# Kernel tuning notes

Measured on AMD Instinct MI355X. Metric: run time of the kernel, lower is better.

## Reference

```python
import jax, jax.numpy as jnp
import numpy as np

DIM = 64
HEADS = 8
DIM_HEAD = 64
INNER = HEADS * DIM_HEAD  # 512
MLP = 256
DEPTH = 4
B = 64
HW = 15
NPATCH = HW * HW  # 225
N = NPATCH + 1    # 226 tokens incl cls
SCALE = DIM_HEAD ** -0.5
EPS = 1e-5


def setup_inputs() -> dict:
    key = jax.random.key(0)
    ks = jax.random.split(key, 20)
    s = 0.02
    inp = {
        "hsi": jax.random.normal(ks[0], (B, DIM, HW, HW), jnp.float32),
        "lidar": jax.random.normal(ks[1], (B, DIM, HW, HW), jnp.float32),
        "cls_hsi": jax.random.normal(ks[2], (1, 1, DIM), jnp.float32),
        "cls_lidar": jax.random.normal(ks[3], (1, 1, DIM), jnp.float32),
        "pos_hsi": jax.random.normal(ks[4], (1, N, DIM), jnp.float32),
        "pos_lidar": jax.random.normal(ks[5], (1, N, DIM), jnp.float32),
        "fmg_w": jax.random.normal(ks[6], (2 * DIM, DIM * DIM), jnp.float32) * s,
        "ln1_g": jnp.ones((DEPTH, DIM), jnp.float32),
        "ln1_b": jnp.zeros((DEPTH, DIM), jnp.float32),
        "qkv_w": jax.random.normal(ks[7], (DEPTH, DIM, 3 * INNER), jnp.float32) * s,
        "out_w": jax.random.normal(ks[8], (DEPTH, INNER, DIM), jnp.float32) * s,
        "out_b": jnp.zeros((DEPTH, DIM), jnp.float32),
        "ln2_g": jnp.ones((DEPTH, DIM), jnp.float32),
        "ln2_b": jnp.zeros((DEPTH, DIM), jnp.float32),
        "ff_w1": jax.random.normal(ks[9], (DEPTH, DIM, MLP), jnp.float32) * s,
        "ff_b1": jnp.zeros((DEPTH, MLP), jnp.float32),
        "ff_w2": jax.random.normal(ks[10], (DEPTH, MLP, DIM), jnp.float32) * s,
        "ff_b2": jnp.zeros((DEPTH, DIM), jnp.float32),
    }
    return inp


def _ln(x, g, b):
    m = x.mean(-1, keepdims=True)
    v = ((x - m) ** 2).mean(-1, keepdims=True)
    return (x - m) * jax.lax.rsqrt(v + EPS) * g + b


def _attn(x, dfm, g, b, wqkv, wo, bo):
    # x: [B, N, DIM]; dfm: [B, DIM_HEAD] diagonal of per-sample fusion matrix
    xn = _ln(x, g, b)
    qkv = xn @ wqkv  # [B, N, 3*INNER]
    q, k, v = jnp.split(qkv, 3, axis=-1)
    def heads(t):
        return t.reshape(B, N, HEADS, DIM_HEAD).transpose(0, 2, 1, 3)  # bhnd
    q, v = heads(q), heads(v)
    # torch.einsum('bhnd,bdd->bhnd', q, fm): repeated 'd' in bdd = diagonal of fm
    k = q * dfm[:, None, None, :]
    dots = jnp.einsum('bhid,bhjd->bhij', q, k) * SCALE
    attn = jax.nn.softmax(dots, axis=-1)
    out = jnp.einsum('bhij,bhjd->bhid', attn, v)
    out = out.transpose(0, 2, 1, 3).reshape(B, N, INNER)
    return out @ wo + bo


def _ff(x, g, b, w1, b1, w2, b2):
    xn = _ln(x, g, b)
    h = jax.nn.gelu(xn @ w1 + b1, approximate=False)
    return h @ w2 + b2


def reference(hsi, lidar, cls_hsi, cls_lidar, pos_hsi, pos_lidar, fmg_w,
              ln1_g, ln1_b, qkv_w, out_w, out_b, ln2_g, ln2_b,
              ff_w1, ff_b1, ff_w2, ff_b2):
    # patch_to_embedding with p1=p2=1: b c h w -> b (h w) c
    h_e = hsi.reshape(B, DIM, NPATCH).transpose(0, 2, 1)
    l_e = lidar.reshape(B, DIM, NPATCH).transpose(0, 2, 1)

    # fusion matrix from pre-exchange embeddings
    x = jnp.concatenate([h_e.mean(1), l_e.mean(1)], axis=-1)  # [B, 2*DIM]
    fm = jax.nn.sigmoid(x @ fmg_w).reshape(B, DIM, DIM)
    dfm = jnp.diagonal(fm, axis1=1, axis2=2)  # [B, DIM]

    # _exchange_embedding (faithful to source: reads both halves from hsi)
    n2 = NPATCH // 2
    h_ex = jnp.concatenate([h_e[:, :n2], h_e[:, n2:]], axis=1)
    l_ex = jnp.concatenate([h_e[:, :n2], h_e[:, n2:]], axis=1)

    h_ex = jnp.concatenate([jnp.broadcast_to(cls_hsi, (B, 1, DIM)), h_ex], axis=1)
    l_ex = jnp.concatenate([jnp.broadcast_to(cls_lidar, (B, 1, DIM)), l_ex], axis=1)
    h_ex = h_ex + pos_hsi[:, :N]
    l_ex = l_ex + pos_lidar[:, :N]

    def run_layers(h, l):
        for i in range(DEPTH):
            h = _attn(h, dfm, ln1_g[i], ln1_b[i], qkv_w[i], out_w[i], out_b[i]) + h
            h = _ff(h, ln2_g[i], ln2_b[i], ff_w1[i], ff_b1[i], ff_w2[i], ff_b2[i]) + h
            l = _attn(l, dfm, ln1_g[i], ln1_b[i], qkv_w[i], out_w[i], out_b[i]) + l
            l = _ff(l, ln2_g[i], ln2_b[i], ff_w1[i], ff_b1[i], ff_w2[i], ff_b2[i]) + l
        return h, l

    h_ex, l_ex = run_layers(h_ex, l_ex)

    # _exchange_token: swap cls tokens
    h_new = jnp.concatenate([l_ex[:, :1], h_ex[:, 1:]], axis=1)
    l_new = jnp.concatenate([h_ex[:, :1], l_ex[:, 1:]], axis=1)

    h_new, l_new = run_layers(h_new, l_new)
    return h_new[:, 0] + l_new[:, 0]
```

## Files before the change

### kernel.cpp

```cpp
#include <hip/hip_runtime.h>
#include <hip/hip_bf16.h>
#include <cstdint>

#define NB 64
#define ND 64
#define NH 8
#define DH 64
#define NIN 512
#define NMLP 256
#define NDEPTH 4
#define NPATCH 225
#define NTOK 226
#define NSB 128
#define NROWS (NSB*NTOK)

#define VP 240

typedef __attribute__((ext_vector_type(8))) short bfrag8;
typedef __attribute__((ext_vector_type(4))) float ffrag4;

__device__ __forceinline__ unsigned short f2b(float f) {
  __hip_bfloat16 h = __float2bfloat16(f);
  unsigned short u; __builtin_memcpy(&u, &h, 2); return u;
}

__global__ void k_dfm(const float* __restrict__ hsi, const float* __restrict__ lidar,
                      const float* __restrict__ fmg_w, float* __restrict__ sdfm) {
  __shared__ float xc[128];
  int b = blockIdx.x, t = threadIdx.x;
  const float* src = (t < 64) ? hsi : lidar;
  int d = t & 63;
  const float* p = src + ((size_t)b * 64 + d) * NPATCH;
  float s = 0.f;
  for (int i = 0; i < NPATCH; ++i) s += p[i];
  xc[t] = s * (1.0f / 225.0f);
  __syncthreads();
  if (t < 64) {
    float acc = 0.f;
    const float* w = fmg_w + t * 65;
    for (int c = 0; c < 128; ++c) acc += xc[c] * w[c * 4096];
    float sg = 1.0f / (1.0f + expf(-acc));
    sdfm[b * 64 + t] = sqrtf(sg);
  }
}

__global__ void k_build(const float* __restrict__ hsi,
                        const float* __restrict__ cls_h, const float* __restrict__ cls_l,
                        const float* __restrict__ pos_h, const float* __restrict__ pos_l,
                        const float* __restrict__ g, const float* __restrict__ bb,
                        float* __restrict__ X, uint16_t* __restrict__ Xn) {
  int r = blockIdx.x;
  int sb = r / NTOK, n = r - sb * NTOK;
  int s = sb >> 6, b = sb & 63;
  int d = threadIdx.x;
  float v;
  if (n == 0) v = s ? cls_l[d] : cls_h[d];
  else        v = hsi[((size_t)b * 64 + d) * NPATCH + (n - 1)];
  v += (s ? pos_l : pos_h)[n * ND + d];
  X[(size_t)r * ND + d] = v;
  float sm = v, sq = v * v;
  #pragma unroll
  for (int o = 32; o; o >>= 1) { sm += __shfl_xor(sm, o); sq += __shfl_xor(sq, o); }
  float m = sm * (1.f / 64.f);
  float rs = rsqrtf(sq * (1.f / 64.f) - m * m + 1e-5f);
  Xn[(size_t)r * ND + d] = f2b((v - m) * rs * g[d] + bb[d]);
}

__global__ __launch_bounds__(256) void k_wconv(
    const float* __restrict__ qkv_w, const float* __restrict__ out_w,
    const float* __restrict__ ff_w1, const float* __restrict__ ff_w2,
    uint16_t* __restrict__ Wqv, uint16_t* __restrict__ Wo,
    uint16_t* __restrict__ W1, uint16_t* __restrict__ W2) {
  int i = blockIdx.x * 256 + threadIdx.x;
  if (i < 262144) {
    int ly = i >> 16, rem = i & 65535, n = rem >> 6, k = rem & 63;
    int col = n + ((n >> 9) << 9);
    Wqv[i] = f2b(qkv_w[((size_t)ly * 64 + k) * 1536 + col]);
  } else if (i < 393216) {
    int j = i - 262144;
    int ly = j >> 15, rem = j & 32767, n = rem >> 9, k = rem & 511;
    Wo[j] = f2b(out_w[((size_t)ly * 512 + k) * 64 + n]);
  } else if (i < 458752) {
    int j = i - 393216;
    int ly = j >> 14, rem = j & 16383, n = rem >> 6, k = rem & 63;
    W1[j] = f2b(ff_w1[((size_t)ly * 64 + k) * 256 + n]);
  } else {
    int j = i - 458752;
    int ly = j >> 14, rem = j & 16383, n = rem >> 8, k = rem & 255;
    W2[j] = f2b(ff_w2[((size_t)ly * 256 + k) * 64 + n]);
  }
}

__global__ __launch_bounds__(256) void k_fattn(const uint16_t* __restrict__ Xn,
    const uint16_t* __restrict__ Wqv,
    const float* __restrict__ sdfm, uint16_t* __restrict__ Og) {
  __shared__ __align__(16) uint16_t qs[240 * 64];
  __shared__ __align__(16) uint16_t vt[64 * VP];
  __shared__ __align__(16) uint16_t pb[4][512];
  int bh = blockIdx.x;
  int sb = bh >> 3, h = bh & 7;
  int t = threadIdx.x, w = t >> 6, l = t & 63;
  int quad = l >> 4, c = l & 15;
  const uint16_t* Xb = Xn + (size_t)sb * NTOK * ND;

  float sf[4];
  #pragma unroll
  for (int dt = 0; dt < 4; ++dt)
    sf[dt] = sdfm[(sb & 63) * 64 + dt * 16 + c] * 0.35355339059327373f;

  for (int it = w; it < 15; it += 4) {
    int i0 = it * 16;
    int ri = i0 + c; if (ri > 225) ri = 225;
    bfrag8 a0 = *(const bfrag8*)(Xb + (size_t)ri * 64 + quad * 8);
    bfrag8 a1 = *(const bfrag8*)(Xb + (size_t)ri * 64 + 32 + quad * 8);
    #pragma unroll
    for (int dt = 0; dt < 4; ++dt) {
      int nq = h * 64 + dt * 16 + c;
      bfrag8 bq0 = *(const bfrag8*)(Wqv + (size_t)nq * 64 + quad * 8);
      bfrag8 bq1 = *(const bfrag8*)(Wqv + (size_t)nq * 64 + 32 + quad * 8);
      ffrag4 zq = {0.f, 0.f, 0.f, 0.f};
      zq = __builtin_amdgcn_mfma_f32_16x16x32_bf16(a0, bq0, zq, 0, 0, 0);
      zq = __builtin_amdgcn_mfma_f32_16x16x32_bf16(a1, bq1, zq, 0, 0, 0);
      bfrag8 bv0 = *(const bfrag8*)(Wqv + (size_t)(512 + nq) * 64 + quad * 8);
      bfrag8 bv1 = *(const bfrag8*)(Wqv + (size_t)(512 + nq) * 64 + 32 + quad * 8);
      ffrag4 zv = {0.f, 0.f, 0.f, 0.f};
      zv = __builtin_amdgcn_mfma_f32_16x16x32_bf16(a0, bv0, zv, 0, 0, 0);
      zv = __builtin_amdgcn_mfma_f32_16x16x32_bf16(a1, bv1, zv, 0, 0, 0);
      int d = dt * 16 + c;
      #pragma unroll
      for (int r = 0; r < 4; ++r) {
        int i = i0 + quad * 4 + r;
        qs[i * 64 + ((((d >> 3) ^ (i & 7))) << 3) + (d & 7)] = f2b(zq[r] * sf[dt]);
        vt[d * VP + i] = f2b(zv[r]);
      }
    }
  }
  __syncthreads();

  uint16_t* pw = &pb[w][0];
  for (int it = w; it < 15; it += 4) {
    int i0 = it * 16;
    int ra = i0 + c, sa = ra & 7;
    bfrag8 a0 = *(const bfrag8*)(qs + ra * 64 + ((quad ^ sa) << 3));
    bfrag8 a1 = *(const bfrag8*)(qs + ra * 64 + (((quad + 4) ^ sa) << 3));
    ffrag4 acc[15];
    #pragma unroll
    for (int jt = 0; jt < 15; ++jt) {
      int rb = jt * 16 + c, sk = rb & 7;
      bfrag8 b0 = *(const bfrag8*)(qs + rb * 64 + ((quad ^ sk) << 3));
      bfrag8 b1 = *(const bfrag8*)(qs + rb * 64 + (((quad + 4) ^ sk) << 3));
      ffrag4 z = {0.f, 0.f, 0.f, 0.f};
      z = __builtin_amdgcn_mfma_f32_16x16x32_bf16(a0, b0, z, 0, 0, 0);
      z = __builtin_amdgcn_mfma_f32_16x16x32_bf16(a1, b1, z, 0, 0, 0);
      acc[jt] = z;
    }
    float rinv[4];
    #pragma unroll
    for (int r = 0; r < 4; ++r) {
      float m = -1e30f;
      #pragma unroll
      for (int jt = 0; jt < 15; ++jt) m = fmaxf(m, acc[jt][r]);
      #pragma unroll
      for (int o = 8; o; o >>= 1) m = fmaxf(m, __shfl_xor(m, o));
      float s = 0.f;
      #pragma unroll
      for (int jt = 0; jt < 15; ++jt) {
        float p = __expf(acc[jt][r] - m);
        if (jt == 14 && c >= 2) p = 0.f;
        acc[jt][r] = p;
        s += p;
      }
      #pragma unroll
      for (int o = 8; o; o >>= 1) s += __shfl_xor(s, o);
      rinv[r] = 1.f / s;
    }
    ffrag4 oa[4];
    #pragma unroll
    for (int dt = 0; dt < 4; ++dt) oa[dt] = (ffrag4){0.f, 0.f, 0.f, 0.f};
    for (int jc = 0; jc < 8; ++jc) {
      if (jc == 7) {
        *(uint64_t*)(pw + c * 32 + 16 + quad * 4) = 0ull;
      }
      #pragma unroll
      for (int r = 0; r < 4; ++r) {
        int row = quad * 4 + r;
        pw[row * 32 + c] = f2b(acc[2 * jc][r] * rinv[r]);
        if (jc < 7) pw[row * 32 + 16 + c] = f2b(acc[2 * jc + 1][r] * rinv[r]);
      }
      bfrag8 pa = *(const bfrag8*)(pw + c * 32 + quad * 8);
      int j0 = jc * 32;
      #pragma unroll
      for (int dt = 0; dt < 4; ++dt) {
        bfrag8 vb;
        if (jc < 7)
          vb = *(const bfrag8*)(vt + (dt * 16 + c) * VP + j0 + quad * 8);
        else
          vb = *(const bfrag8*)(vt + (dt * 16 + c) * VP + 224 + (quad & 1) * 8);
        oa[dt] = __builtin_amdgcn_mfma_f32_16x16x32_bf16(pa, vb, oa[dt], 0, 0, 0);
      }
    }
    #pragma unroll
    for (int dt = 0; dt < 4; ++dt) {
      #pragma unroll
      for (int r = 0; r < 4; ++r) {
        int i = i0 + quad * 4 + r;
        if (i < NTOK)
          Og[((size_t)sb * NTOK + i) * NIN + h * DH + dt * 16 + c] = f2b(oa[dt][r]);
      }
    }
  }
}

__global__ __launch_bounds__(256) void k_proj(const uint16_t* __restrict__ Og,
    const uint16_t* __restrict__ Wot,
    const float* __restrict__ bo, float* __restrict__ X,
    const float* __restrict__ g2, const float* __restrict__ bb2,
    uint16_t* __restrict__ Xn2) {
  int t = threadIdx.x, w = t >> 6, l = t & 63;
  int quad = l >> 4, c = l & 15;
  int r0 = blockIdx.x * 64;
  const uint16_t* orow = Og + (size_t)(r0 + w * 16 + c) * 512 + quad * 8;
  bfrag8 a[16];
  #pragma unroll
  for (int kc = 0; kc < 16; ++kc) a[kc] = *(const bfrag8*)(orow + kc * 32);
  ffrag4 acc[4];
  #pragma unroll
  for (int jt = 0; jt < 4; ++jt) acc[jt] = (ffrag4){0.f, 0.f, 0.f, 0.f};
  #pragma unroll
  for (int kc = 0; kc < 16; ++kc) {
    #pragma unroll
    for (int jt = 0; jt < 4; ++jt) {
      bfrag8 b = *(const bfrag8*)(Wot + (size_t)(jt * 16 + c) * 512 + kc * 32 + quad * 8);
      acc[jt] = __builtin_amdgcn_mfma_f32_16x16x32_bf16(a[kc], b, acc[jt], 0, 0, 0);
    }
  }
  float xv[4][4];
  #pragma unroll
  for (int jt = 0; jt < 4; ++jt) {
    float bv = bo[jt * 16 + c];
    #pragma unroll
    for (int r = 0; r < 4; ++r) {
      int il = w * 16 + quad * 4 + r;
      size_t idx = (size_t)(r0 + il) * 64 + jt * 16 + c;
      float v = X[idx] + acc[jt][r] + bv;
      X[idx] = v;
      xv[jt][r] = v;
    }
  }
  #pragma unroll
  for (int r = 0; r < 4; ++r) {
    float s = xv[0][r] + xv[1][r] + xv[2][r] + xv[3][r];
    float q = xv[0][r]*xv[0][r] + xv[1][r]*xv[1][r] + xv[2][r]*xv[2][r] + xv[3][r]*xv[3][r];
    #pragma unroll
    for (int o = 8; o; o >>= 1) { s += __shfl_xor(s, o); q += __shfl_xor(q, o); }
    float m = s * (1.f / 64.f);
    float rs = rsqrtf(q * (1.f / 64.f) - m * m + 1e-5f);
    int il = w * 16 + quad * 4 + r;
    #pragma unroll
    for (int jt = 0; jt < 4; ++jt) {
      int n = jt * 16 + c;
      Xn2[(size_t)(r0 + il) * 64 + n] = f2b((xv[jt][r] - m) * rs * g2[n] + bb2[n]);
    }
  }
}

__global__ __launch_bounds__(256) void k_ff(float* __restrict__ X,
    const uint16_t* __restrict__ Xn2,
    const uint16_t* __restrict__ W1t,
    const float* __restrict__ b1,
    const uint16_t* __restrict__ W2t,
    const float* __restrict__ b2,
    const float* __restrict__ gn, const float* __restrict__ bbn,
    uint16_t* __restrict__ XnOut) {
  __shared__ __align__(16) uint16_t ha[4][16 * 264];
  int t = threadIdx.x, w = t >> 6, l = t & 63;
  int quad = l >> 4, c = l & 15;
  int r0 = blockIdx.x * 64;
  const uint16_t* xrow = Xn2 + (size_t)(r0 + w * 16 + c) * 64;
  bfrag8 a0 = *(const bfrag8*)(xrow + quad * 8);
  bfrag8 a1 = *(const bfrag8*)(xrow + 32 + quad * 8);
  ffrag4 acc[16];
  #pragma unroll
  for (int jt = 0; jt < 16; ++jt) {
    bfrag8 b0  = *(const bfrag8*)(W1t + (size_t)(jt * 16 + c) * 64 + quad * 8);
    bfrag8 b1f = *(const bfrag8*)(W1t + (size_t)(jt * 16 + c) * 64 + 32 + quad * 8);
    ffrag4 z = {0.f, 0.f, 0.f, 0.f};
    z = __builtin_amdgcn_mfma_f32_16x16x32_bf16(a0, b0, z, 0, 0, 0);
    z = __builtin_amdgcn_mfma_f32_16x16x32_bf16(a1, b1f, z, 0, 0, 0);
    acc[jt] = z;
  }
  uint16_t* haw = &ha[w][0];
  #pragma unroll
  for (int jt = 0; jt < 16; ++jt) {
    float bv = b1[jt * 16 + c];
    #pragma unroll
    for (int r = 0; r < 4; ++r) {
      float z = acc[jt][r] + bv;
      float hg = 0.5f * z * (1.f + erff(z * 0.7071067811865476f));
      haw[(quad * 4 + r) * 264 + jt * 16 + c] = f2b(hg);
    }
  }
  __syncthreads();
  ffrag4 o2[4];
  #pragma unroll
  for (int jt = 0; jt < 4; ++jt) o2[jt] = (ffrag4){0.f, 0.f, 0.f, 0.f};
  #pragma unroll
  for (int kc = 0; kc < 8; ++kc) {
    bfrag8 pa = *(const bfrag8*)(haw + c * 264 + kc * 32 + quad * 8);
    #pragma unroll
    for (int jt = 0; jt < 4; ++jt) {
      bfrag8 vb = *(const bfrag8*)(W2t + (size_t)(jt * 16 + c) * 256 + kc * 32 + quad * 8);
      o2[jt] = __builtin_amdgcn_mfma_f32_16x16x32_bf16(pa, vb, o2[jt], 0, 0, 0);
    }
  }
  float xv[4][4];
  #pragma unroll
  for (int jt = 0; jt < 4; ++jt) {
    float bv = b2[jt * 16 + c];
    #pragma unroll
    for (int r = 0; r < 4; ++r) {
      int il = w * 16 + quad * 4 + r;
      size_t idx = (size_t)(r0 + il) * 64 + jt * 16 + c;
      float v = X[idx] + o2[jt][r] + bv;
      X[idx] = v;
      xv[jt][r] = v;
    }
  }
  #pragma unroll
  for (int r = 0; r < 4; ++r) {
    float s = xv[0][r] + xv[1][r] + xv[2][r] + xv[3][r];
    float q = xv[0][r]*xv[0][r] + xv[1][r]*xv[1][r] + xv[2][r]*xv[2][r] + xv[3][r]*xv[3][r];
    #pragma unroll
    for (int o = 8; o; o >>= 1) { s += __shfl_xor(s, o); q += __shfl_xor(q, o); }
    float m = s * (1.f / 64.f);
    float rs = rsqrtf(q * (1.f / 64.f) - m * m + 1e-5f);
    int il = w * 16 + quad * 4 + r;
    #pragma unroll
    for (int jt = 0; jt < 4; ++jt) {
      int n = jt * 16 + c;
      XnOut[(size_t)(r0 + il) * 64 + n] = f2b((xv[jt][r] - m) * rs * gn[n] + bbn[n]);
    }
  }
}

__global__ void k_xchg(float* __restrict__ X, uint16_t* __restrict__ Xn,
                       const float* __restrict__ g, const float* __restrict__ bb) {
  int b = blockIdx.x, d = threadIdx.x;
  size_t i0 = (size_t)(b * NTOK) * ND + d;
  size_t i1 = (size_t)((64 + b) * NTOK) * ND + d;
  float a = X[i0], cc = X[i1];
  X[i0] = cc; X[i1] = a;
  float s0 = cc, q0 = cc * cc, s1 = a, q1 = a * a;
  #pragma unroll
  for (int o = 32; o; o >>= 1) {
    s0 += __shfl_xor(s0, o); q0 += __shfl_xor(q0, o);
    s1 += __shfl_xor(s1, o); q1 += __shfl_xor(q1, o);
  }
  float m0 = s0 * (1.f / 64.f), rs0 = rsqrtf(q0 * (1.f / 64.f) - m0 * m0 + 1e-5f);
  float m1 = s1 * (1.f / 64.f), rs1 = rsqrtf(q1 * (1.f / 64.f) - m1 * m1 + 1e-5f);
  Xn[i0] = f2b((cc - m0) * rs0 * g[d] + bb[d]);
  Xn[i1] = f2b((a - m1) * rs1 * g[d] + bb[d]);
}

__global__ void k_out(const float* __restrict__ X, float* __restrict__ out) {
  int i = blockIdx.x * 64 + threadIdx.x;
  int b = i >> 6, d = i & 63;
  out[i] = X[(size_t)b * NTOK * ND + d] + X[(size_t)(64 + b) * NTOK * ND + d];
}

extern "C" void kernel_launch(void* const* d_in, const int* in_sizes, int n_in,
                              void* d_out, int out_size, void* d_ws, size_t ws_size,
                              hipStream_t stream) {
  const float* hsi   = (const float*)d_in[0];
  const float* lidar = (const float*)d_in[1];
  const float* cls_h = (const float*)d_in[2];
  const float* cls_l = (const float*)d_in[3];
  const float* pos_h = (const float*)d_in[4];
  const float* pos_l = (const float*)d_in[5];
  const float* fmg_w = (const float*)d_in[6];
  const float* ln1_g = (const float*)d_in[7];
  const float* ln1_b = (const float*)d_in[8];
  const float* qkv_w = (const float*)d_in[9];
  const float* out_w = (const float*)d_in[10];
  const float* out_b = (const float*)d_in[11];
  const float* ln2_g = (const float*)d_in[12];
  const float* ln2_b = (const float*)d_in[13];
  const float* ff_w1 = (const float*)d_in[14];
  const float* ff_b1 = (const float*)d_in[15];
  const float* ff_w2 = (const float*)d_in[16];
  const float* ff_b2 = (const float*)d_in[17];

  char* ws = (char*)d_ws;
  float*    X    = (float*)ws;
  float*    sdfm = (float*)(ws + 7405568);
  uint16_t* Xn   = (uint16_t*)(ws + 7421952);
  uint16_t* Xn2  = (uint16_t*)(ws + 11124736);
  uint16_t* Og   = (uint16_t*)(ws + 14827520);
  uint16_t* Wqv  = (uint16_t*)(ws + 44449792);
  uint16_t* Wo   = (uint16_t*)(ws + 44974080);
  uint16_t* W1   = (uint16_t*)(ws + 45236224);
  uint16_t* W2   = (uint16_t*)(ws + 45367296);

  k_wconv<<<2048, 256, 0, stream>>>(qkv_w, out_w, ff_w1, ff_w2, Wqv, Wo, W1, W2);
  k_dfm<<<NB, 128, 0, stream>>>(hsi, lidar, fmg_w, sdfm);
  k_build<<<NROWS, 64, 0, stream>>>(hsi, cls_h, cls_l, pos_h, pos_l,
                                    ln1_g, ln1_b, X, Xn);
  for (int pass = 0; pass < 2; ++pass) {
    for (int ly = 0; ly < NDEPTH; ++ly) {
      int nx = (ly + 1) & 3;
      k_fattn<<<NSB * NH, 256, 0, stream>>>(Xn, Wqv + (size_t)ly * 65536, sdfm, Og);
      k_proj<<<452, 256, 0, stream>>>(Og, Wo + (size_t)ly * 32768, out_b + ly * ND,
                                      X, ln2_g + ly * ND, ln2_b + ly * ND, Xn2);
      k_ff<<<452, 256, 0, stream>>>(X, Xn2,
                                    W1 + (size_t)ly * 16384, ff_b1 + ly * NMLP,
                                    W2 + (size_t)ly * 16384, ff_b2 + ly * ND,
                                    ln1_g + nx * ND, ln1_b + nx * ND, Xn);
    }
    if (pass == 0) k_xchg<<<64, 64, 0, stream>>>(X, Xn, ln1_g, ln1_b);
  }
  k_out<<<64, 64, 0, stream>>>(X, (float*)d_out);
}
```

Before: 897.8 us.

## Transpose V MFMA, pad V tile, defer softmax normalization, cheaper bf16 convert

The V projection now uses swapped MFMA operands so each lane writes four consecutive d-rows for one token, and the V row pitch grows to 248 so LDS bank conflicts on the transposed store drop. The Q tile shrinks to 226 rows with clamped reads, and the pad columns of V are zeroed explicitly. Softmax normalization moves from every probability element to the final output, and the float-to-bf16 conversion becomes an inline bit-twiddle round-to-nearest-even that does not handle NaN. Together these target LDS traffic and per-element ALU work in the fused attention kernel.

```diff
diff --git a/kernel.cpp b/kernel.cpp
--- a/kernel.cpp
+++ b/kernel.cpp
@@ -14,14 +14,15 @@
 #define NSB 128
 #define NROWS (NSB*NTOK)
 
-#define VP 240
+#define VP 248
 
 typedef __attribute__((ext_vector_type(8))) short bfrag8;
 typedef __attribute__((ext_vector_type(4))) float ffrag4;
 
 __device__ __forceinline__ unsigned short f2b(float f) {
-  __hip_bfloat16 h = __float2bfloat16(f);
-  unsigned short u; __builtin_memcpy(&u, &h, 2); return u;
+  uint32_t u; __builtin_memcpy(&u, &f, 4);
+  u += 0x7fff + ((u >> 16) & 1);
+  return (unsigned short)(u >> 16);
 }
 
 __global__ void k_dfm(const float* __restrict__ hsi, const float* __restrict__ lidar,
@@ -94,7 +95,7 @@
 __global__ __launch_bounds__(256) void k_fattn(const uint16_t* __restrict__ Xn,
     const uint16_t* __restrict__ Wqv,
     const float* __restrict__ sdfm, uint16_t* __restrict__ Og) {
-  __shared__ __align__(16) uint16_t qs[240 * 64];
+  __shared__ __align__(16) uint16_t qs[226 * 64];
   __shared__ __align__(16) uint16_t vt[64 * VP];
   __shared__ __align__(16) uint16_t pb[4][512];
   int bh = blockIdx.x;
@@ -110,9 +111,10 @@
 
   for (int it = w; it < 15; it += 4) {
     int i0 = it * 16;
-    int ri = i0 + c; if (ri > 225) ri = 225;
-    bfrag8 a0 = *(const bfrag8*)(Xb + (size_t)ri * 64 + quad * 8);
-    bfrag8 a1 = *(const bfrag8*)(Xb + (size_t)ri * 64 + 32 + quad * 8);
+    int ric = i0 + c; if (ric > 225) ric = 225;
+    const uint16_t* xr = Xb + (size_t)ric * 64;
+    bfrag8 a0 = *(const bfrag8*)(xr + quad * 8);
+    bfrag8 a1 = *(const bfrag8*)(xr + 32 + quad * 8);
     #pragma unroll
     for (int dt = 0; dt < 4; ++dt) {
       int nq = h * 64 + dt * 16 + c;
@@ -121,32 +123,45 @@
       ffrag4 zq = {0.f, 0.f, 0.f, 0.f};
       zq = __builtin_amdgcn_mfma_f32_16x16x32_bf16(a0, bq0, zq, 0, 0, 0);
       zq = __builtin_amdgcn_mfma_f32_16x16x32_bf16(a1, bq1, zq, 0, 0, 0);
-      bfrag8 bv0 = *(const bfrag8*)(Wqv + (size_t)(512 + nq) * 64 + quad * 8);
-      bfrag8 bv1 = *(const bfrag8*)(Wqv + (size_t)(512 + nq) * 64 + 32 + quad * 8);
-      ffrag4 zv = {0.f, 0.f, 0.f, 0.f};
-      zv = __builtin_amdgcn_mfma_f32_16x16x32_bf16(a0, bv0, zv, 0, 0, 0);
-      zv = __builtin_amdgcn_mfma_f32_16x16x32_bf16(a1, bv1, zv, 0, 0, 0);
       int d = dt * 16 + c;
       #pragma unroll
       for (int r = 0; r < 4; ++r) {
         int i = i0 + quad * 4 + r;
-        qs[i * 64 + ((((d >> 3) ^ (i & 7))) << 3) + (d & 7)] = f2b(zq[r] * sf[dt]);
-        vt[d * VP + i] = f2b(zv[r]);
-      }
-    }
+        if (i < NTOK)
+          qs[i * 64 + ((((d >> 3) ^ (i & 7))) << 3) + (d & 7)] = f2b(zq[r] * sf[dt]);
+      }
+      const uint16_t* wv = Wqv + (size_t)(512 + h * 64 + dt * 16 + c) * 64;
+      bfrag8 av0 = *(const bfrag8*)(wv + quad * 8);
+      bfrag8 av1 = *(const bfrag8*)(wv + 32 + quad * 8);
+      ffrag4 zv = {0.f, 0.f, 0.f, 0.f};
+      zv = __builtin_amdgcn_mfma_f32_16x16x32_bf16(av0, a0, zv, 0, 0, 0);
+      zv = __builtin_amdgcn_mfma_f32_16x16x32_bf16(av1, a1, zv, 0, 0, 0);
+      if (i0 + c < NTOK) {
+        int dd = dt * 16 + quad * 4;
+        #pragma unroll
+        for (int r = 0; r < 4; ++r)
+          vt[(dd + r) * VP + i0 + c] = f2b(zv[r]);
+      }
+    }
+  }
+  for (int idx = t; idx < 64 * 7; idx += 256) {
+    int d = idx / 7, cc = 226 + 2 * (idx % 7);
+    *(uint32_t*)(vt + d * VP + cc) = 0;
   }
   __syncthreads();
 
   uint16_t* pw = &pb[w][0];
   for (int it = w; it < 15; it += 4) {
     int i0 = it * 16;
-    int ra = i0 + c, sa = ra & 7;
+    int ra = i0 + c; if (ra > 225) ra = 225;
+    int sa = ra & 7;
     bfrag8 a0 = *(const bfrag8*)(qs + ra * 64 + ((quad ^ sa) << 3));
     bfrag8 a1 = *(const bfrag8*)(qs + ra * 64 + (((quad + 4) ^ sa) << 3));
     ffrag4 acc[15];
     #pragma unroll
     for (int jt = 0; jt < 15; ++jt) {
-      int rb = jt * 16 + c, sk = rb & 7;
+      int rb = jt * 16 + c; if (rb > 225) rb = 225;
+      int sk = rb & 7;
       bfrag8 b0 = *(const bfrag8*)(qs + rb * 64 + ((quad ^ sk) << 3));
       bfrag8 b1 = *(const bfrag8*)(qs + rb * 64 + (((quad + 4) ^ sk) << 3));
       ffrag4 z = {0.f, 0.f, 0.f, 0.f};
@@ -184,8 +199,8 @@
       #pragma unroll
       for (int r = 0; r < 4; ++r) {
         int row = quad * 4 + r;
-        pw[row * 32 + c] = f2b(acc[2 * jc][r] * rinv[r]);
-        if (jc < 7) pw[row * 32 + 16 + c] = f2b(acc[2 * jc + 1][r] * rinv[r]);
+        pw[row * 32 + c] = f2b(acc[2 * jc][r]);
+        if (jc < 7) pw[row * 32 + 16 + c] = f2b(acc[2 * jc + 1][r]);
       }
       bfrag8 pa = *(const bfrag8*)(pw + c * 32 + quad * 8);
       int j0 = jc * 32;
@@ -205,7 +220,8 @@
       for (int r = 0; r < 4; ++r) {
         int i = i0 + quad * 4 + r;
         if (i < NTOK)
-          Og[((size_t)sb * NTOK + i) * NIN + h * DH + dt * 16 + c] = f2b(oa[dt][r]);
+          Og[((size_t)sb * NTOK + i) * NIN + h * DH + dt * 16 + c] =
+              f2b(oa[dt][r] * rinv[r]);
       }
     }
   }
```

Measured after the change: 940.1 us. 4.7% more time.

## Fold Q·diag·Qᵀ and V·Wo into precomputed per-head matrices; fuse attention with projection

Applied to the files above, without the earlier changes.

Attention is rewritten algebraically. Scores become X·M·Xᵀ, where M = Wq·diag(s)·Wqᵀ is precomputed per layer, batch and head. The value path and output projection fold into G = Wv·Wo, so attention outputs are P·X·G. The separate attention and projection kernels become one mega kernel per (sample, quarter of rows) that loops over heads and writes the residual plus LayerNorm directly, removing the large Og intermediate. The cost is extra precompute kernels, more bf16 roundings of fused products, and a serial head loop with fewer blocks (512).

```diff
diff --git a/kernel.cpp b/kernel.cpp
--- a/kernel.cpp
+++ b/kernel.cpp
@@ -5,23 +5,20 @@
 #define NB 64
 #define ND 64
 #define NH 8
-#define DH 64
-#define NIN 512
-#define NMLP 256
-#define NDEPTH 4
-#define NPATCH 225
 #define NTOK 226
 #define NSB 128
 #define NROWS (NSB*NTOK)
 
-#define VP 240
+#define XTP 232
+#define PWP 40
 
 typedef __attribute__((ext_vector_type(8))) short bfrag8;
 typedef __attribute__((ext_vector_type(4))) float ffrag4;
 
 __device__ __forceinline__ unsigned short f2b(float f) {
-  __hip_bfloat16 h = __float2bfloat16(f);
-  unsigned short u; __builtin_memcpy(&u, &h, 2); return u;
+  uint32_t u; __builtin_memcpy(&u, &f, 4);
+  u += 0x7fff + ((u >> 16) & 1);
+  return (unsigned short)(u >> 16);
 }
 
 __global__ void k_dfm(const float* __restrict__ hsi, const float* __restrict__ lidar,
@@ -30,9 +27,9 @@
   int b = blockIdx.x, t = threadIdx.x;
   const float* src = (t < 64) ? hsi : lidar;
   int d = t & 63;
-  const float* p = src + ((size_t)b * 64 + d) * NPATCH;
+  const float* p = src + ((size_t)b * 64 + d) * 225;
   float s = 0.f;
-  for (int i = 0; i < NPATCH; ++i) s += p[i];
+  for (int i = 0; i < 225; ++i) s += p[i];
   xc[t] = s * (1.0f / 225.0f);
   __syncthreads();
   if (t < 64) {
@@ -55,7 +52,7 @@
   int d = threadIdx.x;
   float v;
   if (n == 0) v = s ? cls_l[d] : cls_h[d];
-  else        v = hsi[((size_t)b * 64 + d) * NPATCH + (n - 1)];
+  else        v = hsi[((size_t)b * 64 + d) * 225 + (n - 1)];
   v += (s ? pos_l : pos_h)[n * ND + d];
   X[(size_t)r * ND + d] = v;
   float sm = v, sq = v * v;
@@ -66,200 +63,223 @@
   Xn[(size_t)r * ND + d] = f2b((v - m) * rs * g[d] + bb[d]);
 }
 
-__global__ __launch_bounds__(256) void k_wconv(
-    const float* __restrict__ qkv_w, const float* __restrict__ out_w,
+__global__ __launch_bounds__(256) void k_wconv2(
     const float* __restrict__ ff_w1, const float* __restrict__ ff_w2,
-    uint16_t* __restrict__ Wqv, uint16_t* __restrict__ Wo,
     uint16_t* __restrict__ W1, uint16_t* __restrict__ W2) {
   int i = blockIdx.x * 256 + threadIdx.x;
-  if (i < 262144) {
-    int ly = i >> 16, rem = i & 65535, n = rem >> 6, k = rem & 63;
-    int col = n + ((n >> 9) << 9);
-    Wqv[i] = f2b(qkv_w[((size_t)ly * 64 + k) * 1536 + col]);
-  } else if (i < 393216) {
-    int j = i - 262144;
-    int ly = j >> 15, rem = j & 32767, n = rem >> 9, k = rem & 511;
-    Wo[j] = f2b(out_w[((size_t)ly * 512 + k) * 64 + n]);
-  } else if (i < 458752) {
-    int j = i - 393216;
-    int ly = j >> 14, rem = j & 16383, n = rem >> 6, k = rem & 63;
-    W1[j] = f2b(ff_w1[((size_t)ly * 64 + k) * 256 + n]);
+  if (i < 65536) {
+    int ly = i >> 14, rem = i & 16383, n = rem >> 6, k = rem & 63;
+    W1[i] = f2b(ff_w1[((size_t)ly * 64 + k) * 256 + n]);
   } else {
-    int j = i - 458752;
+    int j = i - 65536;
     int ly = j >> 14, rem = j & 16383, n = rem >> 8, k = rem & 255;
     W2[j] = f2b(ff_w2[((size_t)ly * 256 + k) * 64 + n]);
   }
 }
 
-__global__ __launch_bounds__(256) void k_fattn(const uint16_t* __restrict__ Xn,
-    const uint16_t* __restrict__ Wqv,
-    const float* __restrict__ sdfm, uint16_t* __restrict__ Og) {
-  __shared__ __align__(16) uint16_t qs[240 * 64];
-  __shared__ __align__(16) uint16_t vt[64 * VP];
-  __shared__ __align__(16) uint16_t pb[4][512];
-  int bh = blockIdx.x;
-  int sb = bh >> 3, h = bh & 7;
-  int t = threadIdx.x, w = t >> 6, l = t & 63;
-  int quad = l >> 4, c = l & 15;
-  const uint16_t* Xb = Xn + (size_t)sb * NTOK * ND;
-
-  float sf[4];
-  #pragma unroll
-  for (int dt = 0; dt < 4; ++dt)
-    sf[dt] = sdfm[(sb & 63) * 64 + dt * 16 + c] * 0.35355339059327373f;
-
-  for (int it = w; it < 15; it += 4) {
-    int i0 = it * 16;
-    int ri = i0 + c; if (ri > 225) ri = 225;
-    bfrag8 a0 = *(const bfrag8*)(Xb + (size_t)ri * 64 + quad * 8);
-    bfrag8 a1 = *(const bfrag8*)(Xb + (size_t)ri * 64 + 32 + quad * 8);
-    #pragma unroll
-    for (int dt = 0; dt < 4; ++dt) {
-      int nq = h * 64 + dt * 16 + c;
-      bfrag8 bq0 = *(const bfrag8*)(Wqv + (size_t)nq * 64 + quad * 8);
-      bfrag8 bq1 = *(const bfrag8*)(Wqv + (size_t)nq * 64 + 32 + quad * 8);
-      ffrag4 zq = {0.f, 0.f, 0.f, 0.f};
-      zq = __builtin_amdgcn_mfma_f32_16x16x32_bf16(a0, bq0, zq, 0, 0, 0);
-      zq = __builtin_amdgcn_mfma_f32_16x16x32_bf16(a1, bq1, zq, 0, 0, 0);
-      bfrag8 bv0 = *(const bfrag8*)(Wqv + (size_t)(512 + nq) * 64 + quad * 8);
-      bfrag8 bv1 = *(const bfrag8*)(Wqv + (size_t)(512 + nq) * 64 + 32 + quad * 8);
-      ffrag4 zv = {0.f, 0.f, 0.f, 0.f};
-      zv = __builtin_amdgcn_mfma_f32_16x16x32_bf16(a0, bv0, zv, 0, 0, 0);
-      zv = __builtin_amdgcn_mfma_f32_16x16x32_bf16(a1, bv1, zv, 0, 0, 0);
-      int d = dt * 16 + c;
-      #pragma unroll
-      for (int r = 0; r < 4; ++r) {
-        int i = i0 + quad * 4 + r;
-        qs[i * 64 + ((((d >> 3) ^ (i & 7))) << 3) + (d & 7)] = f2b(zq[r] * sf[dt]);
-        vt[d * VP + i] = f2b(zv[r]);
-      }
-    }
+__global__ __launch_bounds__(256) void k_gconv(const float* __restrict__ qkv_w,
+    const float* __restrict__ out_w, uint16_t* __restrict__ Gt) {
+  int idx = blockIdx.x * 256 + threadIdx.x;
+  int ly = idx >> 15, h = (idx >> 12) & 7, d = (idx >> 6) & 63, n = idx & 63;
+  const float* qp = qkv_w + ((size_t)(ly * 64 + d)) * 1536 + 1024 + h * 64;
+  const float* op = out_w + ((size_t)(ly * 512 + h * 64)) * 64 + n;
+  float acc = 0.f;
+  for (int dh = 0; dh < 64; ++dh) acc += qp[dh] * op[(size_t)dh * 64];
+  Gt[(((size_t)(ly * 8 + h) * 64 + n) << 6) + d] = f2b(acc);
+}
+
+__global__ void k_mconv(const float* __restrict__ qkv_w,
+    const float* __restrict__ sdfm, uint16_t* __restrict__ Mt) {
+  __shared__ __align__(16) uint16_t ws[64 * 64];
+  int bx = blockIdx.x;
+  int ly = bx >> 9, b = (bx >> 3) & 63, h = bx & 7;
+  int t = threadIdx.x;
+  float sf = sdfm[b * 64 + t] * 0.35355339059327373f;
+  for (int k = 0; k < 64; ++k) {
+    float wv = qkv_w[((size_t)(ly * 64 + k)) * 1536 + h * 64 + t];
+    ws[k * 64 + (((t >> 3) ^ (k & 7)) << 3) + (t & 7)] = f2b(wv * sf);
   }
   __syncthreads();
-
-  uint16_t* pw = &pb[w][0];
-  for (int it = w; it < 15; it += 4) {
-    int i0 = it * 16;
-    int ra = i0 + c, sa = ra & 7;
-    bfrag8 a0 = *(const bfrag8*)(qs + ra * 64 + ((quad ^ sa) << 3));
-    bfrag8 a1 = *(const bfrag8*)(qs + ra * 64 + (((quad + 4) ^ sa) << 3));
-    ffrag4 acc[15];
-    #pragma unroll
-    for (int jt = 0; jt < 15; ++jt) {
+  int quad = t >> 4, c = t & 15;
+  uint16_t* out = Mt + ((size_t)bx << 12);
+  for (int it = 0; it < 4; ++it) {
+    int ra = it * 16 + c, sa = ra & 7;
+    bfrag8 a0 = *(const bfrag8*)(ws + ra * 64 + ((quad ^ sa) << 3));
+    bfrag8 a1 = *(const bfrag8*)(ws + ra * 64 + (((quad + 4) ^ sa) << 3));
+    for (int jt = 0; jt < 4; ++jt) {
       int rb = jt * 16 + c, sk = rb & 7;
-      bfrag8 b0 = *(const bfrag8*)(qs + rb * 64 + ((quad ^ sk) << 3));
-      bfrag8 b1 = *(const bfrag8*)(qs + rb * 64 + (((quad + 4) ^ sk) << 3));
+      bfrag8 b0 = *(const bfrag8*)(ws + rb * 64 + ((quad ^ sk) << 3));
+      bfrag8 b1 = *(const bfrag8*)(ws + rb * 64 + (((quad + 4) ^ sk) << 3));
       ffrag4 z = {0.f, 0.f, 0.f, 0.f};
       z = __builtin_amdgcn_mfma_f32_16x16x32_bf16(a0, b0, z, 0, 0, 0);
       z = __builtin_amdgcn_mfma_f32_16x16x32_bf16(a1, b1, z, 0, 0, 0);
-      acc[jt] = z;
-    }
-    float rinv[4];
-    #pragma unroll
-    for (int r = 0; r < 4; ++r) {
-      float m = -1e30f;
-      #pragma unroll
-      for (int jt = 0; jt < 15; ++jt) m = fmaxf(m, acc[jt][r]);
-      #pragma unroll
-      for (int o = 8; o; o >>= 1) m = fmaxf(m, __shfl_xor(m, o));
-      float s = 0.f;
-      #pragma unroll
-      for (int jt = 0; jt < 15; ++jt) {
-        float p = __expf(acc[jt][r] - m);
-        if (jt == 14 && c >= 2) p = 0.f;
-        acc[jt][r] = p;
-        s += p;
-      }
-      #pragma unroll
-      for (int o = 8; o; o >>= 1) s += __shfl_xor(s, o);
-      rinv[r] = 1.f / s;
-    }
-    ffrag4 oa[4];
-    #pragma unroll
-    for (int dt = 0; dt < 4; ++dt) oa[dt] = (ffrag4){0.f, 0.f, 0.f, 0.f};
-    for (int jc = 0; jc < 8; ++jc) {
-      if (jc == 7) {
-        *(uint64_t*)(pw + c * 32 + 16 + quad * 4) = 0ull;
-      }
-      #pragma unroll
-      for (int r = 0; r < 4; ++r) {
-        int row = quad * 4 + r;
-        pw[row * 32 + c] = f2b(acc[2 * jc][r] * rinv[r]);
-        if (jc < 7) pw[row * 32 + 16 + c] = f2b(acc[2 * jc + 1][r] * rinv[r]);
-      }
-      bfrag8 pa = *(const bfrag8*)(pw + c * 32 + quad * 8);
-      int j0 = jc * 32;
-      #pragma unroll
-      for (int dt = 0; dt < 4; ++dt) {
-        bfrag8 vb;
-        if (jc < 7)
-          vb = *(const bfrag8*)(vt + (dt * 16 + c) * VP + j0 + quad * 8);
-        else
-          vb = *(const bfrag8*)(vt + (dt * 16 + c) * VP + 224 + (quad & 1) * 8);
-        oa[dt] = __builtin_amdgcn_mfma_f32_16x16x32_bf16(pa, vb, oa[dt], 0, 0, 0);
-      }
-    }
-    #pragma unroll
-    for (int dt = 0; dt < 4; ++dt) {
-      #pragma unroll
-      for (int r = 0; r < 4; ++r) {
-        int i = i0 + quad * 4 + r;
-        if (i < NTOK)
-          Og[((size_t)sb * NTOK + i) * NIN + h * DH + dt * 16 + c] = f2b(oa[dt][r]);
-      }
-    }
-  }
-}
-
-__global__ __launch_bounds__(256) void k_proj(const uint16_t* __restrict__ Og,
-    const uint16_t* __restrict__ Wot,
+      #pragma unroll
+      for (int r = 0; r < 4; ++r)
+        out[(it * 16 + quad * 4 + r) * 64 + jt * 16 + c] = f2b(z[r]);
+    }
+  }
+}
+
+__global__ __launch_bounds__(256) void k_mega(const uint16_t* __restrict__ Xn,
+    const uint16_t* __restrict__ Mt,
+    const uint16_t* __restrict__ Gt,
     const float* __restrict__ bo, float* __restrict__ X,
     const float* __restrict__ g2, const float* __restrict__ bb2,
     uint16_t* __restrict__ Xn2) {
-  int t = threadIdx.x, w = t >> 6, l = t & 63;
-  int quad = l >> 4, c = l & 15;
-  int r0 = blockIdx.x * 64;
-  const uint16_t* orow = Og + (size_t)(r0 + w * 16 + c) * 512 + quad * 8;
-  bfrag8 a[16];
-  #pragma unroll
-  for (int kc = 0; kc < 16; ++kc) a[kc] = *(const bfrag8*)(orow + kc * 32);
-  ffrag4 acc[4];
-  #pragma unroll
-  for (int jt = 0; jt < 4; ++jt) acc[jt] = (ffrag4){0.f, 0.f, 0.f, 0.f};
-  #pragma unroll
-  for (int kc = 0; kc < 16; ++kc) {
-    #pragma unroll
-    for (int jt = 0; jt < 4; ++jt) {
-      bfrag8 b = *(const bfrag8*)(Wot + (size_t)(jt * 16 + c) * 512 + kc * 32 + quad * 8);
-      acc[jt] = __builtin_amdgcn_mfma_f32_16x16x32_bf16(a[kc], b, acc[jt], 0, 0, 0);
-    }
-  }
-  float xv[4][4];
-  #pragma unroll
-  for (int jt = 0; jt < 4; ++jt) {
-    float bv = bo[jt * 16 + c];
+  __shared__ __align__(16) uint16_t xt[64 * XTP];
+  __shared__ __align__(16) uint16_t pwb[4][16 * PWP];
+  int bx = blockIdx.x, sb = bx >> 2, qq = bx & 3;
+  int t = threadIdx.x, w = t >> 6, l = t & 63, quad = l >> 4, c = l & 15;
+  const uint16_t* Xb = Xn + (size_t)sb * NTOK * ND;
+
+  for (int idx = t; idx < NTOK * 32; idx += 256) {
+    int j = idx >> 5, d2 = (idx & 31) << 1;
+    uint32_t v = *(const uint32_t*)(Xb + j * 64 + d2);
+    xt[d2 * XTP + j]       = (uint16_t)v;
+    xt[(d2 + 1) * XTP + j] = (uint16_t)(v >> 16);
+  }
+  for (int idx = t; idx < 64 * 3; idx += 256) {
+    int d = idx / 3, cc = 226 + 2 * (idx % 3);
+    *(uint32_t*)(xt + d * XTP + cc) = 0;
+  }
+  __syncthreads();
+
+  int it = qq * 4 + w;
+  if (it <= 14) {
+    int i0 = it * 16;
+    int ric = i0 + c; if (ric > 225) ric = 225;
+    bfrag8 aXg0 = *(const bfrag8*)(Xb + (size_t)ric * 64 + quad * 8);
+    bfrag8 aXg1 = *(const bfrag8*)(Xb + (size_t)ric * 64 + 32 + quad * 8);
+    uint16_t* pw = &pwb[w][0];
+    ffrag4 Oacc[4];
+    #pragma unroll
+    for (int dt = 0; dt < 4; ++dt) Oacc[dt] = (ffrag4){0.f, 0.f, 0.f, 0.f};
+    const uint16_t* Mb = Mt + ((size_t)(sb & 63) << 15);
+
+    for (int h = 0; h < 8; ++h) {
+      const uint16_t* Mh = Mb + ((size_t)h << 12);
+      ffrag4 tacc[4];
+      #pragma unroll
+      for (int dt = 0; dt < 4; ++dt) {
+        bfrag8 b0 = *(const bfrag8*)(Mh + (dt * 16 + c) * 64 + quad * 8);
+        bfrag8 b1 = *(const bfrag8*)(Mh + (dt * 16 + c) * 64 + 32 + quad * 8);
+        ffrag4 z = {0.f, 0.f, 0.f, 0.f};
+        z = __builtin_amdgcn_mfma_f32_16x16x32_bf16(aXg0, b0, z, 0, 0, 0);
+        z = __builtin_amdgcn_mfma_f32_16x16x32_bf16(aXg1, b1, z, 0, 0, 0);
+        tacc[dt] = z;
+      }
+      bfrag8 aT0, aT1;
+      #pragma unroll
+      for (int half = 0; half < 2; ++half) {
+        #pragma unroll
+        for (int d2 = 0; d2 < 2; ++d2)
+          #pragma unroll
+          for (int r = 0; r < 4; ++r)
+            pw[(quad * 4 + r) * PWP + d2 * 16 + c] = f2b(tacc[half * 2 + d2][r]);
+        bfrag8 v = *(const bfrag8*)(pw + c * PWP + quad * 8);
+        if (half == 0) aT0 = v; else aT1 = v;
+      }
+      ffrag4 sacc[15];
+      #pragma unroll
+      for (int jt = 0; jt < 15; ++jt) {
+        int rj = jt * 16 + c; if (rj > 225) rj = 225;
+        bfrag8 b0 = *(const bfrag8*)(Xb + (size_t)rj * 64 + quad * 8);
+        bfrag8 b1 = *(const bfrag8*)(Xb + (size_t)rj * 64 + 32 + quad * 8);
+        ffrag4 z = {0.f, 0.f, 0.f, 0.f};
+        z = __builtin_amdgcn_mfma_f32_16x16x32_bf16(aT0, b0, z, 0, 0, 0);
+        z = __builtin_amdgcn_mfma_f32_16x16x32_bf16(aT1, b1, z, 0, 0, 0);
+        sacc[jt] = z;
+      }
+      float rinv[4];
+      #pragma unroll
+      for (int r = 0; r < 4; ++r) {
+        float m = -1e30f;
+        #pragma unroll
+        for (int jt = 0; jt < 15; ++jt) m = fmaxf(m, sacc[jt][r]);
+        #pragma unroll
+        for (int o = 8; o; o >>= 1) m = fmaxf(m, __shfl_xor(m, o));
+        float s = 0.f;
+        #pragma unroll
+        for (int jt = 0; jt < 15; ++jt) {
+          float p = __expf(sacc[jt][r] - m);
+          if (jt == 14 && c >= 2) p = 0.f;
+          sacc[jt][r] = p;
+          s += p;
+        }
+        #pragma unroll
+        for (int o = 8; o; o >>= 1) s += __shfl_xor(s, o);
+        rinv[r] = 1.f / s;
+      }
+      ffrag4 uacc[4];
+      #pragma unroll
+      for (int dt = 0; dt < 4; ++dt) uacc[dt] = (ffrag4){0.f, 0.f, 0.f, 0.f};
+      #pragma unroll
+      for (int jc = 0; jc < 8; ++jc) {
+        #pragma unroll
+        for (int r = 0; r < 4; ++r) {
+          int row = quad * 4 + r;
+          pw[row * PWP + c] = f2b(sacc[2 * jc][r]);
+          uint16_t hi = 0;
+          if (jc < 7) hi = f2b(sacc[2 * jc + 1][r]);
+          pw[row * PWP + 16 + c] = hi;
+        }
+        bfrag8 pa = *(const bfrag8*)(pw + c * PWP + quad * 8);
+        int jb = (jc < 7) ? (jc * 32 + quad * 8) : 224;
+        #pragma unroll
+        for (int dt = 0; dt < 4; ++dt) {
+          bfrag8 vb = *(const bfrag8*)(xt + (dt * 16 + c) * XTP + jb);
+          uacc[dt] = __builtin_amdgcn_mfma_f32_16x16x32_bf16(pa, vb, uacc[dt], 0, 0, 0);
+        }
+      }
+      const uint16_t* Gh = Gt + ((size_t)h << 12);
+      #pragma unroll
+      for (int half = 0; half < 2; ++half) {
+        #pragma unroll
+        for (int d2 = 0; d2 < 2; ++d2)
+          #pragma unroll
+          for (int r = 0; r < 4; ++r)
+            pw[(quad * 4 + r) * PWP + d2 * 16 + c] = f2b(uacc[half * 2 + d2][r] * rinv[r]);
+        bfrag8 aU = *(const bfrag8*)(pw + c * PWP + quad * 8);
+        #pragma unroll
+        for (int dt = 0; dt < 4; ++dt) {
+          bfrag8 gb = *(const bfrag8*)(Gh + (dt * 16 + c) * 64 + half * 32 + quad * 8);
+          Oacc[dt] = __builtin_amdgcn_mfma_f32_16x16x32_bf16(aU, gb, Oacc[dt], 0, 0, 0);
+        }
+      }
+    }
+
+    float xv[4][4];
+    #pragma unroll
+    for (int dt = 0; dt < 4; ++dt) {
+      float bv = bo[dt * 16 + c];
+      #pragma unroll
+      for (int r = 0; r < 4; ++r) {
+        int i = i0 + quad * 4 + r;
+        float v = 0.f;
+        if (i < NTOK) {
+          size_t idx = ((size_t)sb * NTOK + i) * 64 + dt * 16 + c;
+          v = X[idx] + Oacc[dt][r] + bv;
+          X[idx] = v;
+        }
+        xv[dt][r] = v;
+      }
+    }
     #pragma unroll
     for (int r = 0; r < 4; ++r) {
-      int il = w * 16 + quad * 4 + r;
-      size_t idx = (size_t)(r0 + il) * 64 + jt * 16 + c;
-      float v = X[idx] + acc[jt][r] + bv;
-      X[idx] = v;
-      xv[jt][r] = v;
-    }
-  }
-  #pragma unroll
-  for (int r = 0; r < 4; ++r) {
-    float s = xv[0][r] + xv[1][r] + xv[2][r] + xv[3][r];
-    float q = xv[0][r]*xv[0][r] + xv[1][r]*xv[1][r] + xv[2][r]*xv[2][r] + xv[3][r]*xv[3][r];
-    #pragma unroll
-    for (int o = 8; o; o >>= 1) { s += __shfl_xor(s, o); q += __shfl_xor(q, o); }
-    float m = s * (1.f / 64.f);
-    float rs = rsqrtf(q * (1.f / 64.f) - m * m + 1e-5f);
-    int il = w * 16 + quad * 4 + r;
-    #pragma unroll
-    for (int jt = 0; jt < 4; ++jt) {
-      int n = jt * 16 + c;
-      Xn2[(size_t)(r0 + il) * 64 + n] = f2b((xv[jt][r] - m) * rs * g2[n] + bb2[n]);
+      int i = i0 + quad * 4 + r;
+      float s = xv[0][r] + xv[1][r] + xv[2][r] + xv[3][r];
+      float q = xv[0][r]*xv[0][r] + xv[1][r]*xv[1][r] + xv[2][r]*xv[2][r] + xv[3][r]*xv[3][r];
+      #pragma unroll
+      for (int o = 8; o; o >>= 1) { s += __shfl_xor(s, o); q += __shfl_xor(q, o); }
+      float m = s * (1.f / 64.f);
+      float rs = rsqrtf(q * (1.f / 64.f) - m * m + 1e-5f);
+      if (i < NTOK) {
+        #pragma unroll
+        for (int dt = 0; dt < 4; ++dt) {
+          int n = dt * 16 + c;
+          Xn2[((size_t)sb * NTOK + i) * 64 + n] = f2b((xv[dt][r] - m) * rs * g2[n] + bb2[n]);
+        }
+      }
     }
   }
 }
@@ -395,24 +415,25 @@
   float*    sdfm = (float*)(ws + 7405568);
   uint16_t* Xn   = (uint16_t*)(ws + 7421952);
   uint16_t* Xn2  = (uint16_t*)(ws + 11124736);
-  uint16_t* Og   = (uint16_t*)(ws + 14827520);
-  uint16_t* Wqv  = (uint16_t*)(ws + 44449792);
-  uint16_t* Wo   = (uint16_t*)(ws + 44974080);
-  uint16_t* W1   = (uint16_t*)(ws + 45236224);
-  uint16_t* W2   = (uint16_t*)(ws + 45367296);
-
-  k_wconv<<<2048, 256, 0, stream>>>(qkv_w, out_w, ff_w1, ff_w2, Wqv, Wo, W1, W2);
+  uint16_t* Mt   = (uint16_t*)(ws + 14827520);
+  uint16_t* Gt   = (uint16_t*)(ws + 31604736);
+  uint16_t* W1   = (uint16_t*)(ws + 31866880);
+  uint16_t* W2   = (uint16_t*)(ws + 31997952);
+
+  k_wconv2<<<512, 256, 0, stream>>>(ff_w1, ff_w2, W1, W2);
+  k_gconv<<<512, 256, 0, stream>>>(qkv_w, out_w, Gt);
   k_dfm<<<NB, 128, 0, stream>>>(hsi, lidar, fmg_w, sdfm);
+  k_mconv<<<2048, 64, 0, stream>>>(qkv_w, sdfm, Mt);
   k_build<<<NROWS, 64, 0, stream>>>(hsi, cls_h, cls_l, pos_h, pos_l,
                                     ln1_g, ln1_b, X, Xn);
   for (int pass = 0; pass < 2; ++pass) {
-    for (int ly = 0; ly < NDEPTH; ++ly) {
+    for (int ly = 0; ly < 4; ++ly) {
       int nx = (ly + 1) & 3;
-      k_fattn<<<NSB * NH, 256, 0, stream>>>(Xn, Wqv + (size_t)ly * 65536, sdfm, Og);
-      k_proj<<<452, 256, 0, stream>>>(Og, Wo + (size_t)ly * 32768, out_b + ly * ND,
+      k_mega<<<512, 256, 0, stream>>>(Xn, Mt + (size_t)ly * 2097152,
+                                      Gt + (size_t)ly * 32768, out_b + ly * ND,
                                       X, ln2_g + ly * ND, ln2_b + ly * ND, Xn2);
       k_ff<<<452, 256, 0, stream>>>(X, Xn2,
-                                    W1 + (size_t)ly * 16384, ff_b1 + ly * NMLP,
+                                    W1 + (size_t)ly * 16384, ff_b1 + ly * 256,
                                     W2 + (size_t)ly * 16384, ff_b2 + ly * ND,
                                     ln1_g + nx * ND, ln1_b + nx * ND, Xn);
     }
```

Result: slower. 1.269 ms (+41.4%).

## Fuse out-projection and feed-forward kernels, defer softmax normalization to output

Applied to the files above, without the earlier changes.

Merges k_proj and k_ff into a single k_pf kernel that keeps the LayerNorm2 output in shared memory instead of round-tripping Xn2 through global memory, and drops one launch per layer. In the attention kernel, softmax normalization moves from each probability element to the final output accumulator. f2b is replaced by a manual round-to-nearest-even bit conversion, which skips NaN handling. The block now uses more shared memory, which may reduce occupancy. The __syncthreads is removed, which is safe only because each wave reads just its own region of ha.

```diff
diff --git a/kernel.cpp b/kernel.cpp
--- a/kernel.cpp
+++ b/kernel.cpp
@@ -20,8 +20,9 @@
 typedef __attribute__((ext_vector_type(4))) float ffrag4;
 
 __device__ __forceinline__ unsigned short f2b(float f) {
-  __hip_bfloat16 h = __float2bfloat16(f);
-  unsigned short u; __builtin_memcpy(&u, &h, 2); return u;
+  uint32_t u; __builtin_memcpy(&u, &f, 4);
+  u += 0x7fff + ((u >> 16) & 1);
+  return (unsigned short)(u >> 16);
 }
 
 __global__ void k_dfm(const float* __restrict__ hsi, const float* __restrict__ lidar,
@@ -184,8 +185,8 @@
       #pragma unroll
       for (int r = 0; r < 4; ++r) {
         int row = quad * 4 + r;
-        pw[row * 32 + c] = f2b(acc[2 * jc][r] * rinv[r]);
-        if (jc < 7) pw[row * 32 + 16 + c] = f2b(acc[2 * jc + 1][r] * rinv[r]);
+        pw[row * 32 + c] = f2b(acc[2 * jc][r]);
+        if (jc < 7) pw[row * 32 + 16 + c] = f2b(acc[2 * jc + 1][r]);
       }
       bfrag8 pa = *(const bfrag8*)(pw + c * 32 + quad * 8);
       int j0 = jc * 32;
@@ -205,20 +206,29 @@
       for (int r = 0; r < 4; ++r) {
         int i = i0 + quad * 4 + r;
         if (i < NTOK)
-          Og[((size_t)sb * NTOK + i) * NIN + h * DH + dt * 16 + c] = f2b(oa[dt][r]);
-      }
-    }
-  }
-}
-
-__global__ __launch_bounds__(256) void k_proj(const uint16_t* __restrict__ Og,
+          Og[((size_t)sb * NTOK + i) * NIN + h * DH + dt * 16 + c] =
+              f2b(oa[dt][r] * rinv[r]);
+      }
+    }
+  }
+}
+
+__global__ __launch_bounds__(256) void k_pf(const uint16_t* __restrict__ Og,
     const uint16_t* __restrict__ Wot,
     const float* __restrict__ bo, float* __restrict__ X,
     const float* __restrict__ g2, const float* __restrict__ bb2,
-    uint16_t* __restrict__ Xn2) {
+    const uint16_t* __restrict__ W1t,
+    const float* __restrict__ b1,
+    const uint16_t* __restrict__ W2t,
+    const float* __restrict__ b2,
+    const float* __restrict__ gn, const float* __restrict__ bbn,
+    uint16_t* __restrict__ XnOut) {
+  __shared__ __align__(16) uint16_t xa2[64 * 72];
+  __shared__ __align__(16) uint16_t ha[4][16 * 264];
   int t = threadIdx.x, w = t >> 6, l = t & 63;
   int quad = l >> 4, c = l & 15;
   int r0 = blockIdx.x * 64;
+
   const uint16_t* orow = Og + (size_t)(r0 + w * 16 + c) * 512 + quad * 8;
   bfrag8 a[16];
   #pragma unroll
@@ -259,27 +269,13 @@
     #pragma unroll
     for (int jt = 0; jt < 4; ++jt) {
       int n = jt * 16 + c;
-      Xn2[(size_t)(r0 + il) * 64 + n] = f2b((xv[jt][r] - m) * rs * g2[n] + bb2[n]);
-    }
-  }
-}
-
-__global__ __launch_bounds__(256) void k_ff(float* __restrict__ X,
-    const uint16_t* __restrict__ Xn2,
-    const uint16_t* __restrict__ W1t,
-    const float* __restrict__ b1,
-    const uint16_t* __restrict__ W2t,
-    const float* __restrict__ b2,
-    const float* __restrict__ gn, const float* __restrict__ bbn,
-    uint16_t* __restrict__ XnOut) {
-  __shared__ __align__(16) uint16_t ha[4][16 * 264];
-  int t = threadIdx.x, w = t >> 6, l = t & 63;
-  int quad = l >> 4, c = l & 15;
-  int r0 = blockIdx.x * 64;
-  const uint16_t* xrow = Xn2 + (size_t)(r0 + w * 16 + c) * 64;
+      xa2[il * 72 + n] = f2b((xv[jt][r] - m) * rs * g2[n] + bb2[n]);
+    }
+  }
+  const uint16_t* xrow = xa2 + (w * 16 + c) * 72;
   bfrag8 a0 = *(const bfrag8*)(xrow + quad * 8);
   bfrag8 a1 = *(const bfrag8*)(xrow + 32 + quad * 8);
-  ffrag4 acc[16];
+  ffrag4 acc1[16];
   #pragma unroll
   for (int jt = 0; jt < 16; ++jt) {
     bfrag8 b0  = *(const bfrag8*)(W1t + (size_t)(jt * 16 + c) * 64 + quad * 8);
@@ -287,7 +283,7 @@
     ffrag4 z = {0.f, 0.f, 0.f, 0.f};
     z = __builtin_amdgcn_mfma_f32_16x16x32_bf16(a0, b0, z, 0, 0, 0);
     z = __builtin_amdgcn_mfma_f32_16x16x32_bf16(a1, b1f, z, 0, 0, 0);
-    acc[jt] = z;
+    acc1[jt] = z;
   }
   uint16_t* haw = &ha[w][0];
   #pragma unroll
@@ -295,12 +291,11 @@
     float bv = b1[jt * 16 + c];
     #pragma unroll
     for (int r = 0; r < 4; ++r) {
-      float z = acc[jt][r] + bv;
+      float z = acc1[jt][r] + bv;
       float hg = 0.5f * z * (1.f + erff(z * 0.7071067811865476f));
       haw[(quad * 4 + r) * 264 + jt * 16 + c] = f2b(hg);
     }
   }
-  __syncthreads();
   ffrag4 o2[4];
   #pragma unroll
   for (int jt = 0; jt < 4; ++jt) o2[jt] = (ffrag4){0.f, 0.f, 0.f, 0.f};
@@ -313,7 +308,7 @@
       o2[jt] = __builtin_amdgcn_mfma_f32_16x16x32_bf16(pa, vb, o2[jt], 0, 0, 0);
     }
   }
-  float xv[4][4];
+  float yv[4][4];
   #pragma unroll
   for (int jt = 0; jt < 4; ++jt) {
     float bv = b2[jt * 16 + c];
@@ -323,13 +318,13 @@
       size_t idx = (size_t)(r0 + il) * 64 + jt * 16 + c;
       float v = X[idx] + o2[jt][r] + bv;
       X[idx] = v;
-      xv[jt][r] = v;
+      yv[jt][r] = v;
     }
   }
   #pragma unroll
   for (int r = 0; r < 4; ++r) {
-    float s = xv[0][r] + xv[1][r] + xv[2][r] + xv[3][r];
-    float q = xv[0][r]*xv[0][r] + xv[1][r]*xv[1][r] + xv[2][r]*xv[2][r] + xv[3][r]*xv[3][r];
+    float s = yv[0][r] + yv[1][r] + yv[2][r] + yv[3][r];
+    float q = yv[0][r]*yv[0][r] + yv[1][r]*yv[1][r] + yv[2][r]*yv[2][r] + yv[3][r]*yv[3][r];
     #pragma unroll
     for (int o = 8; o; o >>= 1) { s += __shfl_xor(s, o); q += __shfl_xor(q, o); }
     float m = s * (1.f / 64.f);
@@ -338,7 +333,7 @@
     #pragma unroll
     for (int jt = 0; jt < 4; ++jt) {
       int n = jt * 16 + c;
-      XnOut[(size_t)(r0 + il) * 64 + n] = f2b((xv[jt][r] - m) * rs * gn[n] + bbn[n]);
+      XnOut[(size_t)(r0 + il) * 64 + n] = f2b((yv[jt][r] - m) * rs * gn[n] + bbn[n]);
     }
   }
 }
@@ -394,12 +389,11 @@
   float*    X    = (float*)ws;
   float*    sdfm = (float*)(ws + 7405568);
   uint16_t* Xn   = (uint16_t*)(ws + 7421952);
-  uint16_t* Xn2  = (uint16_t*)(ws + 11124736);
-  uint16_t* Og   = (uint16_t*)(ws + 14827520);
-  uint16_t* Wqv  = (uint16_t*)(ws + 44449792);
-  uint16_t* Wo   = (uint16_t*)(ws + 44974080);
-  uint16_t* W1   = (uint16_t*)(ws + 45236224);
-  uint16_t* W2   = (uint16_t*)(ws + 45367296);
+  uint16_t* Og   = (uint16_t*)(ws + 11124736);
+  uint16_t* Wqv  = (uint16_t*)(ws + 40747008);
+  uint16_t* Wo   = (uint16_t*)(ws + 41271296);
+  uint16_t* W1   = (uint16_t*)(ws + 41533440);
+  uint16_t* W2   = (uint16_t*)(ws + 41664512);
 
   k_wconv<<<2048, 256, 0, stream>>>(qkv_w, out_w, ff_w1, ff_w2, Wqv, Wo, W1, W2);
   k_dfm<<<NB, 128, 0, stream>>>(hsi, lidar, fmg_w, sdfm);
@@ -409,9 +403,8 @@
     for (int ly = 0; ly < NDEPTH; ++ly) {
       int nx = (ly + 1) & 3;
       k_fattn<<<NSB * NH, 256, 0, stream>>>(Xn, Wqv + (size_t)ly * 65536, sdfm, Og);
-      k_proj<<<452, 256, 0, stream>>>(Og, Wo + (size_t)ly * 32768, out_b + ly * ND,
-                                      X, ln2_g + ly * ND, ln2_b + ly * ND, Xn2);
-      k_ff<<<452, 256, 0, stream>>>(X, Xn2,
+      k_pf<<<452, 256, 0, stream>>>(Og, Wo + (size_t)ly * 32768, out_b + ly * ND,
+                                    X, ln2_g + ly * ND, ln2_b + ly * ND,
                                     W1 + (size_t)ly * 16384, ff_b1 + ly * NMLP,
                                     W2 + (size_t)ly * 16384, ff_b2 + ly * ND,
                                     ln1_g + nx * ND, ln1_b + nx * ND, Xn);
```

New measurement: 851.4 us. 5.2% less time.
